# Optimization experiments

Measured on AMD Instinct MI355X. Metric: run time of the kernel, lower is better.

The kernel has to match this reference:

```python
import jax, jax.numpy as jnp
import numpy as np

L = 32        # label_num = len(label2idx)
SOS = 0       # label2idx['[SOS]']
END = 1       # label2idx['[END]']
NEG = -10000.0
B, T = 512, 1024


def setup_inputs() -> dict:
    key = jax.random.key(0)
    k1, k2, k3 = jax.random.split(key, 3)
    emission = jax.random.normal(k1, (B, T, L), dtype=jnp.float32)
    label_ids = jax.random.randint(k2, (B, T), 0, L)
    transitions = jax.random.normal(k3, (L, L), dtype=jnp.float32)
    # CrfLayer.__init__: forbid transitions into [SOS] and out of [END]
    transitions = transitions.at[SOS, :].set(NEG).at[:, END].set(NEG)
    return {"emission": emission, "label_ids": label_ids, "transitions": transitions}


def reference(emission, label_ids, transitions):
    b, t, l = emission.shape
    # ---- _forward_alg: log-partition via sequential logsumexp recurrence ----
    alpha0 = jnp.full((b, l), NEG, dtype=emission.dtype).at[:, SOS].set(0.0)
    feats_t = jnp.transpose(emission, (1, 0, 2))  # [T, B, L]

    def step(alpha, feat):
        # aa[b, j, i] = alpha[b, i] + feat[b, j] + transitions[j, i]
        aa = alpha[:, None, :] + feat[:, :, None] + transitions[None, :, :]
        return jax.nn.logsumexp(aa, axis=2), None

    alpha, _ = jax.lax.scan(step, alpha0, feats_t)
    forward_score = jax.nn.logsumexp(alpha + transitions[END][None, :], axis=1)  # [B]

    # ---- _score_sentence: score of the gold path ----
    tags = jnp.concatenate(
        [jnp.full((b, 1), SOS, dtype=label_ids.dtype), label_ids], axis=1)  # [B, T+1]
    trans_score = transitions[tags[:, 1:], tags[:, :-1]].sum(axis=1)          # [B]
    emit_score = jnp.take_along_axis(
        emission, tags[:, 1:, None].astype(jnp.int32), axis=2)[..., 0].sum(axis=1)  # [B]
    gold_score = trans_score + emit_score + transitions[END, tags[:, -1]]

    # loss = sum(forward_score - gold_score)
    return jnp.sum(forward_score - gold_score)
```

## Files before the change

kernel.cpp:

```cpp
#include <hip/hip_runtime.h>


typedef float  f32x16 __attribute__((ext_vector_type(16)));
typedef short  s16x8  __attribute__((ext_vector_type(8)));

#define TT 1024
#define LL 32
#define BB 512
#define NC 8
#define CL 128
#define MS 33

union Frag { s16x8 v; unsigned u[4]; };

__device__ __forceinline__ unsigned pack_bf16(float lo, float hi) {
    return __builtin_amdgcn_perm(__float_as_uint(hi), __float_as_uint(lo), 0x07060302u);
}

__global__ __launch_bounds__(NC * 64, 4) void crf_fused_kernel(
    const float* __restrict__ emission,
    const int*   __restrict__ label_ids,
    const float* __restrict__ transitions,
    float*       __restrict__ out)
{
    __shared__ __align__(16) float shM[NC][32 * MS];
    __shared__ float shQ[2][64];
    __shared__ float tgArr[NC];
    __shared__ int   capArr[NC];

    const int tid  = threadIdx.x;
    const int w    = tid >> 6;
    const int lane = tid & 63;
    const int j    = lane & 31;
    const int h    = lane >> 5;
    const int b    = blockIdx.x;
    const int t0   = w * CL;

    const int*   labB = label_ids + b * TT + t0;
    const float* emB  = emission + ((size_t)b * TT + t0) * LL + j;

    {
        float g = 0.0f;
#pragma unroll
        for (int u = 0; u < 2; ++u) {
            int tt = t0 + 64 * u + lane;
            int l1 = labB[64 * u + lane];
            int l0 = (tt == 0) ? 0 : label_ids[b * TT + tt - 1];
            g += transitions[(l1 << 5) + l0];
            g += emission[((size_t)b * TT + tt) * LL + l1];
            if (tt == TT - 1) g += transitions[32 + l1];
        }
#pragma unroll
        for (int m = 32; m >= 1; m >>= 1) g += __shfl_xor(g, m, 64);
        if (lane == 0) tgArr[w] = g;
    }

    const float* trow = transitions + j * 32;
    float E0[8], E1[8];
#pragma unroll
    for (int i = 0; i < 8; ++i) {
        int col = (i & 3) + 8 * (i >> 2) + 4 * h;
        E0[i] = __expf(trow[col]);
        E1[i] = __expf(trow[16 + col]);
    }

    Frag B0, B1;
#pragma unroll
    for (int i = 0; i < 8; ++i) {
        int row = (i & 3) + 8 * (i >> 2) + 4 * h;
        B0.v[i] = (short)((row == j)      ? 0x3F80 : 0);
        B1.v[i] = (short)((row + 16 == j) ? 0x3F80 : 0);
    }

    f32x16 zc, acc;
#pragma unroll
    for (int i = 0; i < 16; ++i) zc[i] = 0.0f;

    float ring[8];
#pragma unroll
    for (int s = 0; s < 8; ++s) ring[s] = emB[s * LL];

    float sc = 1.0f;
    int   Cap = 0, elast = 0;

    for (int s0 = 0; s0 < CL; s0 += 8) {
#pragma unroll
        for (int k = 0; k < 8; ++k) {
            const int s = s0 + k;
            float feat = ring[k];

            float fs = ((k & 3) == 0) ? (__expf(feat) * sc) : __expf(feat);

            Frag A0, A1;
#pragma unroll
            for (int p = 0; p < 4; ++p) {
                A0.u[p] = pack_bf16(fs * E0[2 * p], fs * E0[2 * p + 1]);
                A1.u[p] = pack_bf16(fs * E1[2 * p], fs * E1[2 * p + 1]);
            }

            acc = __builtin_amdgcn_mfma_f32_32x32x16_bf16(A0.v, B0.v, zc, 0, 0, 0);
            acc = __builtin_amdgcn_mfma_f32_32x32x16_bf16(A1.v, B1.v, acc, 0, 0, 0);

            if ((k & 3) == 3) {
                int pb = __builtin_amdgcn_readlane(__float_as_int(acc[2]), 0);
                int e  = ((pb >> 23) & 0xff) - 127;
                sc = __int_as_float((127 - e) << 23);
                Cap += e;
                elast = e;
            }

            int nf = s + 8; nf = (nf < CL) ? nf : (CL - 1);
            ring[k] = emB[nf * LL];

#pragma unroll
            for (int p = 0; p < 4; ++p) {
                B0.u[p] = pack_bf16(acc[2 * p],     acc[2 * p + 1]);
                B1.u[p] = pack_bf16(acc[8 + 2 * p], acc[9 + 2 * p]);
            }
        }
    }
    Cap -= elast;

#pragma unroll
    for (int r = 0; r < 16; ++r) {
        int row = (r & 3) + 8 * (r >> 2) + 4 * h;
        shM[w][row * MS + j] = acc[r];
    }
    if (lane == 0) capArr[w] = Cap;

    __syncthreads();

    if (w == 0) {
        const float Eend = __expf(transitions[32 + j]);
        float q = (j == 0) ? 1.0f : 0.0f;
        int   Cq = 0;
        float gold = 0.0f;

#pragma unroll
        for (int c = 0; c < NC; ++c) {
            shQ[c & 1][lane] = q;
            asm volatile("s_waitcnt lgkmcnt(0)" ::: "memory");
            __builtin_amdgcn_wave_barrier();
            const float* Mrow = &shM[c][j * MS];
            const float* qv   = &shQ[c & 1][h * 32];
            float a0 = 0.f, a1 = 0.f, a2 = 0.f, a3 = 0.f;
#pragma unroll
            for (int i = 0; i < 32; i += 4) {
                a0 = fmaf(Mrow[i],     qv[i],     a0);
                a1 = fmaf(Mrow[i + 1], qv[i + 1], a1);
                a2 = fmaf(Mrow[i + 2], qv[i + 2], a2);
                a3 = fmaf(Mrow[i + 3], qv[i + 3], a3);
            }
            float qn = (a0 + a1) + (a2 + a3);
            int pb = __builtin_amdgcn_readlane(__float_as_int(qn), 2);
            int e  = ((pb >> 23) & 0xff) - 127;
            qn *= __int_as_float((127 - e) << 23);
            Cq += e + capArr[c];
            gold += tgArr[c];
            q = qn;
        }

        float v = q * Eend;
#pragma unroll
        for (int m = 16; m >= 1; m >>= 1) v += __shfl_xor(v, m, 32);
        float fwd = __logf(v) + (float)Cq * 0.69314718055994531f;

        if (lane == 0) atomicAdd(out, fwd - gold);
    }
}

extern "C" void kernel_launch(void* const* d_in, const int* in_sizes, int n_in,
                              void* d_out, int out_size, void* d_ws, size_t ws_size,
                              hipStream_t stream)
{
    const float* emission    = (const float*)d_in[0];
    const int*   label_ids   = (const int*)d_in[1];
    const float* transitions = (const float*)d_in[2];
    float* out = (float*)d_out;

    hipMemsetAsync(out, 0, sizeof(float), stream);
    crf_fused_kernel<<<BB, NC * 64, 0, stream>>>(emission, label_ids, transitions, out);
}
```

Measured before the change: 137.5 us.

## Interleave two independent chunk recurrences per wave to hide MFMA latency

Each wave now owns two 64-step sub-chunks of its 128-step span instead of one 128-step chain, and advances both recurrences in lockstep. The two chains are independent, so their MFMA, bf16 packing and rescale work can overlap and hide the dependent-chain latency of the serial scan. In exchange each wave holds twice the accumulators and fragments, which raises register pressure. The final combine wave now walks 16 transfer matrices instead of 8, and LDS use for shM doubles.

Result: slower. 156.9 us (+14.1%).

```diff
diff --git a/kernel.cpp b/kernel.cpp
--- a/kernel.cpp
+++ b/kernel.cpp
@@ -7,8 +7,8 @@
 #define TT 1024
 #define LL 32
 #define BB 512
-#define NC 8
-#define CL 128
+#define NC 16
+#define CL 64
 #define MS 33
 
 union Frag { s16x8 v; unsigned u[4]; };
@@ -17,7 +17,7 @@
     return __builtin_amdgcn_perm(__float_as_uint(hi), __float_as_uint(lo), 0x07060302u);
 }
 
-__global__ __launch_bounds__(NC * 64, 4) void crf_fused_kernel(
+__global__ __launch_bounds__(512, 4) void crf_fused_kernel(
     const float* __restrict__ emission,
     const int*   __restrict__ label_ids,
     const float* __restrict__ transitions,
@@ -25,7 +25,7 @@
 {
     __shared__ __align__(16) float shM[NC][32 * MS];
     __shared__ float shQ[2][64];
-    __shared__ float tgArr[NC];
+    __shared__ float tgArr[8];
     __shared__ int   capArr[NC];
 
     const int tid  = threadIdx.x;
@@ -34,7 +34,7 @@
     const int j    = lane & 31;
     const int h    = lane >> 5;
     const int b    = blockIdx.x;
-    const int t0   = w * CL;
+    const int t0   = w * (2 * CL);
 
     const int*   labB = label_ids + b * TT + t0;
     const float* emB  = emission + ((size_t)b * TT + t0) * LL + j;
@@ -64,69 +64,79 @@
         E1[i] = __expf(trow[16 + col]);
     }
 
-    Frag B0, B1;
+    Frag B0[2], B1[2];
 #pragma unroll
     for (int i = 0; i < 8; ++i) {
         int row = (i & 3) + 8 * (i >> 2) + 4 * h;
-        B0.v[i] = (short)((row == j)      ? 0x3F80 : 0);
-        B1.v[i] = (short)((row + 16 == j) ? 0x3F80 : 0);
+        short id0 = (short)((row == j)      ? 0x3F80 : 0);
+        short id1 = (short)((row + 16 == j) ? 0x3F80 : 0);
+        B0[0].v[i] = id0; B1[0].v[i] = id1;
+        B0[1].v[i] = id0; B1[1].v[i] = id1;
     }
 
-    f32x16 zc, acc;
+    f32x16 zc, acc[2];
 #pragma unroll
     for (int i = 0; i < 16; ++i) zc[i] = 0.0f;
 
-    float ring[8];
+    float ring[2][8];
 #pragma unroll
-    for (int s = 0; s < 8; ++s) ring[s] = emB[s * LL];
+    for (int s = 0; s < 8; ++s) {
+        ring[0][s] = emB[s * LL];
+        ring[1][s] = emB[(CL + s) * LL];
+    }
 
-    float sc = 1.0f;
-    int   Cap = 0, elast = 0;
+    float sc[2] = {1.0f, 1.0f};
+    int   Cap[2] = {0, 0}, elast[2] = {0, 0};
 
     for (int s0 = 0; s0 < CL; s0 += 8) {
 #pragma unroll
         for (int k = 0; k < 8; ++k) {
             const int s = s0 + k;
-            float feat = ring[k];
+            const int nf = (s + 8 < CL) ? (s + 8) : (CL - 1);
+#pragma unroll
+            for (int q = 0; q < 2; ++q) {
+                float feat = ring[q][k];
+                float fs = ((k & 3) == 0) ? (__expf(feat) * sc[q]) : __expf(feat);
 
-            float fs = ((k & 3) == 0) ? (__expf(feat) * sc) : __expf(feat);
+                Frag A0, A1;
+#pragma unroll
+                for (int p = 0; p < 4; ++p) {
+                    A0.u[p] = pack_bf16(fs * E0[2 * p], fs * E0[2 * p + 1]);
+                    A1.u[p] = pack_bf16(fs * E1[2 * p], fs * E1[2 * p + 1]);
+                }
 
-            Frag A0, A1;
-#pragma unroll
-            for (int p = 0; p < 4; ++p) {
-                A0.u[p] = pack_bf16(fs * E0[2 * p], fs * E0[2 * p + 1]);
-                A1.u[p] = pack_bf16(fs * E1[2 * p], fs * E1[2 * p + 1]);
-            }
+                acc[q] = __builtin_amdgcn_mfma_f32_32x32x16_bf16(A0.v, B0[q].v, zc, 0, 0, 0);
+                acc[q] = __builtin_amdgcn_mfma_f32_32x32x16_bf16(A1.v, B1[q].v, acc[q], 0, 0, 0);
 
-            acc = __builtin_amdgcn_mfma_f32_32x32x16_bf16(A0.v, B0.v, zc, 0, 0, 0);
-            acc = __builtin_amdgcn_mfma_f32_32x32x16_bf16(A1.v, B1.v, acc, 0, 0, 0);
+                if ((k & 3) == 3) {
+                    int pb = __builtin_amdgcn_readlane(__float_as_int(acc[q][2]), 0);
+                    int e  = ((pb >> 23) & 0xff) - 127;
+                    sc[q] = __int_as_float((127 - e) << 23);
+                    Cap[q] += e;
+                    elast[q] = e;
+                }
 
-            if ((k & 3) == 3) {
-                int pb = __builtin_amdgcn_readlane(__float_as_int(acc[2]), 0);
-                int e  = ((pb >> 23) & 0xff) - 127;
-                sc = __int_as_float((127 - e) << 23);
-                Cap += e;
-                elast = e;
-            }
-
-            int nf = s + 8; nf = (nf < CL) ? nf : (CL - 1);
-            ring[k] = emB[nf * LL];
+                ring[q][k] = emB[(q * CL + nf) * LL];
 
 #pragma unroll
-            for (int p = 0; p < 4; ++p) {
-                B0.u[p] = pack_bf16(acc[2 * p],     acc[2 * p + 1]);
-                B1.u[p] = pack_bf16(acc[8 + 2 * p], acc[9 + 2 * p]);
+                for (int p = 0; p < 4; ++p) {
+                    B0[q].u[p] = pack_bf16(acc[q][2 * p],     acc[q][2 * p + 1]);
+                    B1[q].u[p] = pack_bf16(acc[q][8 + 2 * p], acc[q][9 + 2 * p]);
+                }
             }
         }
     }
-    Cap -= elast;
 
 #pragma unroll
-    for (int r = 0; r < 16; ++r) {
-        int row = (r & 3) + 8 * (r >> 2) + 4 * h;
-        shM[w][row * MS + j] = acc[r];
+    for (int q = 0; q < 2; ++q) {
+        Cap[q] -= elast[q];
+#pragma unroll
+        for (int r = 0; r < 16; ++r) {
+            int row = (r & 3) + 8 * (r >> 2) + 4 * h;
+            shM[2 * w + q][row * MS + j] = acc[q][r];
+        }
+        if (lane == 0) capArr[2 * w + q] = Cap[q];
     }
-    if (lane == 0) capArr[w] = Cap;
 
     __syncthreads();
 
@@ -134,7 +144,6 @@
         const float Eend = __expf(transitions[32 + j]);
         float q = (j == 0) ? 1.0f : 0.0f;
         int   Cq = 0;
-        float gold = 0.0f;
 
 #pragma unroll
         for (int c = 0; c < NC; ++c) {
@@ -156,7 +165,6 @@
             int e  = ((pb >> 23) & 0xff) - 127;
             qn *= __int_as_float((127 - e) << 23);
             Cq += e + capArr[c];
-            gold += tgArr[c];
             q = qn;
         }
 
@@ -164,6 +172,10 @@
 #pragma unroll
         for (int m = 16; m >= 1; m >>= 1) v += __shfl_xor(v, m, 32);
         float fwd = __logf(v) + (float)Cq * 0.69314718055994531f;
+
+        float gold = 0.0f;
+#pragma unroll
+        for (int c = 0; c < 8; ++c) gold += tgArr[c];
 
         if (lane == 0) atomicAdd(out, fwd - gold);
     }
@@ -179,5 +191,5 @@
     float* out = (float*)d_out;
 
     hipMemsetAsync(out, 0, sizeof(float), stream);
-    crf_fused_kernel<<<BB, NC * 64, 0, stream>>>(emission, label_ids, transitions, out);
+    crf_fused_kernel<<<BB, 512, 0, stream>>>(emission, label_ids, transitions, out);
 }
```
